# Kernel optimization log

Measured on AMD Instinct MI355X. Metric: run time of the kernel, lower is better.

Reference implementation:

```python
import jax, jax.numpy as jnp
import numpy as np

C = 512
NUM_HEADS = 8
GROUPS = 32
EPS = 1e-5


def setup_inputs() -> dict:
    key = jax.random.key(0)
    ks = jax.random.split(key, 7)
    B, H, W = 8, 32, 32
    x = jax.random.normal(ks[0], (B, C, H, W), dtype=jnp.float32)
    gn_w = jnp.ones((C,), dtype=jnp.float32)
    gn_b = jnp.zeros((C,), dtype=jnp.float32)
    # 1x1 convs as dense matrices [out, in]
    qkv_w = jax.random.normal(ks[1], (3 * C, C), dtype=jnp.float32) * (1.0 / np.sqrt(C))
    qkv_b = jnp.zeros((3 * C,), dtype=jnp.float32)
    proj_w = jax.random.normal(ks[2], (C, C), dtype=jnp.float32) * (1.0 / np.sqrt(C))
    proj_b = jnp.zeros((C,), dtype=jnp.float32)
    return {"x": x, "gn_w": gn_w, "gn_b": gn_b, "qkv_w": qkv_w,
            "qkv_b": qkv_b, "proj_w": proj_w, "proj_b": proj_b}


def reference(x, gn_w, gn_b, qkv_w, qkv_b, proj_w, proj_b):
    B, Cc, H, W = x.shape
    nh = NUM_HEADS
    d = Cc // nh
    N = H * W

    # GroupNorm(32, C) with affine
    xg = x.reshape(B, GROUPS, Cc // GROUPS, H, W)
    mean = jnp.mean(xg, axis=(2, 3, 4), keepdims=True)
    var = jnp.var(xg, axis=(2, 3, 4), keepdims=True)
    hn = ((xg - mean) * jax.lax.rsqrt(var + EPS)).reshape(B, Cc, H, W)
    hn = hn * gn_w[None, :, None, None] + gn_b[None, :, None, None]

    # 1x1 conv QKV projection: [B, 3C, H, W]
    qkv = jnp.einsum('oc,bchw->bohw', qkv_w, hn) + qkv_b[None, :, None, None]
    q, k, v = jnp.split(qkv, 3, axis=1)

    def to_heads(t):  # [B, C, H, W] -> [B, nh, N, d]
        return t.reshape(B, nh, d, N).transpose(0, 1, 3, 2)

    q, k, v = to_heads(q), to_heads(k), to_heads(v)
    scale = d ** (-0.5)
    attn = jax.nn.softmax(jnp.einsum('bhnd,bhmd->bhnm', q, k) * scale, axis=-1)
    o = jnp.einsum('bhnm,bhmd->bhnd', attn, v)          # [B, nh, N, d]
    o = o.transpose(0, 1, 3, 2).reshape(B, Cc, H, W)

    # 1x1 conv output projection + residual
    o = jnp.einsum('oc,bchw->bohw', proj_w, o) + proj_b[None, :, None, None]
    return x + o
```

## Files before the change

kernel.cpp:

```cpp
#include <hip/hip_runtime.h>

typedef __bf16 bf16x8 __attribute__((ext_vector_type(8)));
typedef float f32x4 __attribute__((ext_vector_type(4)));

#define MFMA(a, b, c) __builtin_amdgcn_mfma_f32_16x16x32_bf16(a, b, c, 0, 0, 0)

#define CS 0.18033688011112042f

__device__ __forceinline__ ushort f2bf(float f) {
    __bf16 h = (__bf16)f;
    return *(ushort*)&h;
}
__device__ __forceinline__ float bf2f(ushort u) {
    unsigned int x = ((unsigned int)u) << 16;
    return __uint_as_float(x);
}

__device__ __forceinline__ void stage_tile64(ushort* lds, const ushort* gbase,
                                             int row_stride, int nchunks,
                                             int wave, int lane) {
    int r8 = lane >> 3;
    int cswz = ((lane & 7) ^ r8) << 4;
#pragma unroll
    for (int c = wave; c < nchunks; c += 4) {
        const char* g = (const char*)(gbase + (size_t)(c * 8 + r8) * row_stride) + cswz;
        __builtin_amdgcn_global_load_lds(
            (const __attribute__((address_space(1))) unsigned int*)g,
            (__attribute__((address_space(3))) unsigned int*)((char*)lds + c * 1024),
            16, 0, 0);
    }
}

__device__ __forceinline__ void stage_tile64w2(ushort* lds, const ushort* gbase,
                                               int row_stride, int nchunks,
                                               int wave, int lane) {
    int r8 = lane >> 3;
    int cswz = ((lane & 7) ^ r8) << 4;
#pragma unroll
    for (int c = wave; c < nchunks; c += 2) {
        const char* g = (const char*)(gbase + (size_t)(c * 8 + r8) * row_stride) + cswz;
        __builtin_amdgcn_global_load_lds(
            (const __attribute__((address_space(1))) unsigned int*)g,
            (__attribute__((address_space(3))) unsigned int*)((char*)lds + c * 1024),
            16, 0, 0);
    }
}

__device__ __forceinline__ bf16x8 lds_read_row(const ushort* lds, int row, int cb) {
    return *(const bf16x8*)((const char*)lds + row * 128 + (cb ^ ((row & 7) << 4)));
}

__device__ __forceinline__ void stage_tile32(ushort* lds, const ushort* gbase,
                                             int row_stride, int nchunks,
                                             int wave, int lane) {
    int r16 = lane >> 2;
    int csw = (((lane & 3) ^ ((lane >> 3) & 3)) << 3);
#pragma unroll
    for (int c = wave; c < nchunks; c += 4) {
        const ushort* g = gbase + (size_t)(c * 16 + r16) * row_stride + csw;
        __builtin_amdgcn_global_load_lds(
            (const __attribute__((address_space(1))) unsigned int*)g,
            (__attribute__((address_space(3))) unsigned int*)((char*)lds + c * 1024),
            16, 0, 0);
    }
}

__device__ __forceinline__ bf16x8 lds_read_row32(const ushort* lds, int row, int cb) {
    return *(const bf16x8*)((const char*)lds + row * 64 + (cb ^ (((row >> 1) & 3) << 4)));
}

__global__ __launch_bounds__(256) void gn_cvt_kernel(const float* __restrict__ x,
                                                     const float* __restrict__ gnw,
                                                     const float* __restrict__ gnb,
                                                     ushort* __restrict__ hnT,
                                                     const float* __restrict__ w1,
                                                     const float* __restrict__ w2,
                                                     ushort* __restrict__ o1,
                                                     ushort* __restrict__ o2) {
    __shared__ ushort xcache[16 * 1028];
    __shared__ float red[8];
    __shared__ float sw[16], sb[16];

    if (blockIdx.x >= 256) {
        int t = (blockIdx.x - 256) * 256 + threadIdx.x;
        const int n1q = (1536 * 512) / 4;
        float4 v;
        ushort* dst;
        int idx;
        if (t < n1q) {
            v = ((const float4*)w1)[t]; dst = o1; idx = t;
        } else {
            idx = t - n1q;
            v = ((const float4*)w2)[idx]; dst = o2;
        }
        ushort4 p;
        p.x = f2bf(v.x); p.y = f2bf(v.y); p.z = f2bf(v.z); p.w = f2bf(v.w);
        ((ushort4*)dst)[idx] = p;
        return;
    }

    int b = blockIdx.x >> 5, g = blockIdx.x & 31;
    const float* xp = x + (size_t)(b * 512 + g * 16) * 1024;
    int t = threadIdx.x;

    float s = 0.f, ss = 0.f;
    const float4* xp4 = (const float4*)xp;
    for (int i = t; i < 4096; i += 256) {
        float4 v = xp4[i];
        s += (v.x + v.y) + (v.z + v.w);
        ss += (v.x * v.x + v.y * v.y) + (v.z * v.z + v.w * v.w);
        int f = i * 4;
        int cc = f >> 10, nl = f & 1023;
        ushort4 c;
        c.x = f2bf(v.x); c.y = f2bf(v.y); c.z = f2bf(v.z); c.w = f2bf(v.w);
        *(ushort4*)&xcache[cc * 1028 + nl] = c;
    }
#pragma unroll
    for (int off = 32; off >= 1; off >>= 1) {
        s += __shfl_xor(s, off);
        ss += __shfl_xor(ss, off);
    }
    int wave = t >> 6;
    if ((t & 63) == 0) { red[wave] = s; red[wave + 4] = ss; }
    if (t < 16) { sw[t] = gnw[g * 16 + t]; sb[t] = gnb[g * 16 + t]; }
    __syncthreads();
    float S = red[0] + red[1] + red[2] + red[3];
    float SS = red[4] + red[5] + red[6] + red[7];
    float mean = S * (1.0f / 16384.0f);
    float var = SS * (1.0f / 16384.0f) - mean * mean;
    float rstd = rsqrtf(var + 1e-5f);

    int cc0 = (t & 3) * 4;
    int nb = t >> 2;
    float w0 = sw[cc0] * rstd, w1_ = sw[cc0 + 1] * rstd,
          w2_ = sw[cc0 + 2] * rstd, w3 = sw[cc0 + 3] * rstd;
    float b0 = sb[cc0] - mean * w0, b1 = sb[cc0 + 1] - mean * w1_,
          b2 = sb[cc0 + 2] - mean * w2_, b3 = sb[cc0 + 3] - mean * w3;
#pragma unroll
    for (int k = 0; k < 16; ++k) {
        int nl = nb + 64 * k;
        ushort4 p;
        p.x = f2bf(bf2f(xcache[(cc0 + 0) * 1028 + nl]) * w0 + b0);
        p.y = f2bf(bf2f(xcache[(cc0 + 1) * 1028 + nl]) * w1_ + b1);
        p.z = f2bf(bf2f(xcache[(cc0 + 2) * 1028 + nl]) * w2_ + b2);
        p.w = f2bf(bf2f(xcache[(cc0 + 3) * 1028 + nl]) * w3 + b3);
        *(ushort4*)(hnT + ((size_t)b * 1024 + nl) * 512 + g * 16 + cc0) = p;
    }
}

__global__ __launch_bounds__(256, 3) void gemm_qkv(const ushort* __restrict__ Wb,
                                                   const ushort* __restrict__ hnT,
                                                   const float* __restrict__ qkvb,
                                                   ushort* __restrict__ qT,
                                                   ushort* __restrict__ kT,
                                                   ushort* __restrict__ vb) {
    int lane = threadIdx.x & 63, wave = threadIdx.x >> 6;
    int l15 = lane & 15, lg = lane >> 4;
    int bi = blockIdx.x;
    int b = bi & 7;
    int slot = bi >> 3;
    int m0 = (slot % 12) * 128;
    int n0 = (slot / 12) * 128;
    int mw = (wave >> 1) * 64, nw = (wave & 1) * 64;
    const ushort* Ag = Wb + (size_t)m0 * 512;
    const ushort* Bg = hnT + (size_t)b * 524288 + (size_t)n0 * 512;

    __shared__ ushort abuf[3][4096];
    __shared__ ushort bbuf[3][4096];

    f32x4 acc[4][4] = {};
#pragma unroll
    for (int p = 0; p < 2; ++p) {
        stage_tile32(abuf[p], Ag + p * 32, 512, 8, wave, lane);
        stage_tile32(bbuf[p], Bg + p * 32, 512, 8, wave, lane);
    }
    asm volatile("s_waitcnt vmcnt(4)" ::: "memory");
    __builtin_amdgcn_s_barrier();

    int cur = 0;
#pragma unroll 1
    for (int t = 0; t < 16; ++t) {
        if (t < 14) {
            int nxt = cur + 2; if (nxt >= 3) nxt -= 3;
            stage_tile32(abuf[nxt], Ag + (t + 2) * 32, 512, 8, wave, lane);
            stage_tile32(bbuf[nxt], Bg + (t + 2) * 32, 512, 8, wave, lane);
        }
        const ushort* A = abuf[cur];
        const ushort* B = bbuf[cur];
        bf16x8 af[4], bfr[4];
#pragma unroll
        for (int i = 0; i < 4; i++)
            af[i] = lds_read_row32(A, mw + i * 16 + l15, lg * 16);
#pragma unroll
        for (int j = 0; j < 4; j++)
            bfr[j] = lds_read_row32(B, nw + j * 16 + l15, lg * 16);
        __builtin_amdgcn_s_setprio(1);
#pragma unroll
        for (int i = 0; i < 4; i++)
#pragma unroll
            for (int j = 0; j < 4; j++)
                acc[i][j] = MFMA(af[i], bfr[j], acc[i][j]);
        __builtin_amdgcn_s_setprio(0);
        if (t < 15) {
            if (t < 14) asm volatile("s_waitcnt vmcnt(4)" ::: "memory");
            else        asm volatile("s_waitcnt vmcnt(0)" ::: "memory");
            __builtin_amdgcn_s_barrier();
        }
        cur = cur + 1; if (cur == 3) cur = 0;
    }

#pragma unroll
    for (int i = 0; i < 4; i++) {
        int ob = m0 + mw + i * 16 + lg * 4;
        float bias[4];
#pragma unroll
        for (int r = 0; r < 4; r++) bias[r] = qkvb[ob + r];
        int part = ob >> 9;
        int oo = ob & 511;
#pragma unroll
        for (int j = 0; j < 4; j++) {
            int n = n0 + nw + j * 16 + l15;
            if (part == 2) {
                int L = n & 63;
                int cf = L >> 4;
                int s = ((cf >> 1) << 5) | (((L >> 2) & 3) << 3) | ((cf & 1) << 2) | (L & 3);
                int np = (n & ~63) | s;
#pragma unroll
                for (int r = 0; r < 4; r++)
                    vb[(size_t)(b * 512 + oo + r) * 1024 + np] = f2bf(acc[i][j][r] + bias[r]);
            } else {
                ushort* dst = part ? kT : qT;
                float sc = part ? 1.0f : CS;
                int h = oo >> 6, dd = oo & 63;
                ushort4 p;
                p.x = f2bf((acc[i][j][0] + bias[0]) * sc);
                p.y = f2bf((acc[i][j][1] + bias[1]) * sc);
                p.z = f2bf((acc[i][j][2] + bias[2]) * sc);
                p.w = f2bf((acc[i][j][3] + bias[3]) * sc);
                *(ushort4*)(dst + ((size_t)((b * 8 + h) * 1024 + n)) * 64 + dd) = p;
            }
        }
    }
}

__global__ __launch_bounds__(128) void attn_kernel(const ushort* __restrict__ qT,
                                                   const ushort* __restrict__ kT,
                                                   const ushort* __restrict__ vb,
                                                   ushort* __restrict__ aoT) {
    int bi = blockIdx.x;
    int bh = ((bi >> 6) << 3) | (bi & 7);
    int q0 = ((bi >> 3) & 7) * 128;
    int b = bh >> 3, h = bh & 7;
    int lane = threadIdx.x & 63, wave = threadIdx.x >> 6;
    int l15 = lane & 15, lg = lane >> 4;
    const ushort* qp = qT + (size_t)bh * 65536;
    const ushort* kp = kT + (size_t)bh * 65536;
    const ushort* vp = vb + (size_t)bh * 65536;

    __shared__ ushort kbuf[3][4096];
    __shared__ ushort vbuf[3][4096];

    bf16x8 vone;
#pragma unroll
    for (int e = 0; e < 8; e++) vone[e] = (__bf16)1.0f;

    int qbase = q0 + wave * 64;
    bf16x8 qf[4][2];
#pragma unroll
    for (int i = 0; i < 4; i++)
#pragma unroll
        for (int kh = 0; kh < 2; kh++)
            qf[i][kh] = *(const bf16x8*)(qp + (size_t)(qbase + i * 16 + l15) * 64 + kh * 32 + lg * 8);

    f32x4 oacc[4][4] = {};
    f32x4 lacc[4] = {};

    stage_tile64w2(kbuf[0], kp, 64, 8, wave, lane);
    stage_tile64w2(vbuf[0], vp, 1024, 8, wave, lane);
    stage_tile64w2(kbuf[1], kp + 4096, 64, 8, wave, lane);
    stage_tile64w2(vbuf[1], vp + 64, 1024, 8, wave, lane);
    asm volatile("s_waitcnt vmcnt(8)" ::: "memory");
    __builtin_amdgcn_s_barrier();

    int cur = 0;
#pragma unroll 1
    for (int t = 0; t < 16; ++t) {
        if (t < 14) {
            int nxt = cur + 2; if (nxt >= 3) nxt -= 3;
            stage_tile64w2(kbuf[nxt], kp + (size_t)(t + 2) * 4096, 64, 8, wave, lane);
            stage_tile64w2(vbuf[nxt], vp + (t + 2) * 64, 1024, 8, wave, lane);
        }
        const ushort* kb = kbuf[cur];
        const ushort* vc = vbuf[cur];

        bf16x8 kf[2][4], vf[2][4];
#pragma unroll
        for (int kh = 0; kh < 2; kh++)
#pragma unroll
            for (int cf = 0; cf < 4; cf++)
                kf[kh][cf] = lds_read_row(kb, cf * 16 + l15, kh * 64 + lg * 16);
#pragma unroll
        for (int ks = 0; ks < 2; ks++)
#pragma unroll
            for (int cf = 0; cf < 4; cf++)
                vf[ks][cf] = lds_read_row(vc, cf * 16 + l15, ks * 64 + lg * 16);

#pragma unroll
        for (int ih = 0; ih < 2; ih++) {
            f32x4 sacc[2][4] = {};
            __builtin_amdgcn_s_setprio(1);
#pragma unroll
            for (int kh = 0; kh < 2; kh++)
#pragma unroll
                for (int cf = 0; cf < 4; cf++) {
                    sacc[0][cf] = MFMA(kf[kh][cf], qf[2 * ih + 0][kh], sacc[0][cf]);
                    sacc[1][cf] = MFMA(kf[kh][cf], qf[2 * ih + 1][kh], sacc[1][cf]);
                }
            __builtin_amdgcn_s_setprio(0);

            bf16x8 pa[2][2];
#pragma unroll
            for (int ii = 0; ii < 2; ii++)
#pragma unroll
                for (int ks = 0; ks < 2; ks++) {
                    bf16x8 tr;
#pragma unroll
                    for (int jhi = 0; jhi < 2; jhi++)
#pragma unroll
                        for (int r = 0; r < 4; r++)
                            tr[jhi * 4 + r] = (__bf16)exp2f(sacc[ii][ks * 2 + jhi][r]);
                    pa[ii][ks] = tr;
                }

            __builtin_amdgcn_s_setprio(1);
#pragma unroll
            for (int ii = 0; ii < 2; ii++)
#pragma unroll
                for (int ks = 0; ks < 2; ks++) {
                    lacc[2 * ih + ii] = MFMA(pa[ii][ks], vone, lacc[2 * ih + ii]);
#pragma unroll
                    for (int cf = 0; cf < 4; cf++)
                        oacc[2 * ih + ii][cf] = MFMA(pa[ii][ks], vf[ks][cf], oacc[2 * ih + ii][cf]);
                }
            __builtin_amdgcn_s_setprio(0);
        }

        if (t < 15) {
            if (t < 14) asm volatile("s_waitcnt vmcnt(8)" ::: "memory");
            else        asm volatile("s_waitcnt vmcnt(0)" ::: "memory");
            __builtin_amdgcn_s_barrier();
        }
        cur = cur + 1; if (cur == 3) cur = 0;
    }

#pragma unroll
    for (int i = 0; i < 4; i++)
#pragma unroll
        for (int r = 0; r < 4; r++) {
            float inv = 1.0f / lacc[i][r];
            int n = qbase + i * 16 + lg * 4 + r;
            size_t obase = ((size_t)b * 1024 + n) * 512 + h * 64;
#pragma unroll
            for (int cf = 0; cf < 4; cf++)
                aoT[obase + cf * 16 + l15] = f2bf(oacc[i][cf][r] * inv);
        }
}

__global__ __launch_bounds__(256) void gemm_proj(const ushort* __restrict__ Wb,
                                                 const ushort* __restrict__ aoT,
                                                 const float* __restrict__ projb,
                                                 const float* __restrict__ x,
                                                 float* __restrict__ out) {
    int lane = threadIdx.x & 63, wave = threadIdx.x >> 6;
    int l15 = lane & 15, lg = lane >> 4;
    int bi = blockIdx.x;
    int b = bi & 7;
    int slot = bi >> 3;
    int m0 = (slot & 3) * 128;
    int n0 = (slot >> 2) * 64;
    int mw = (wave >> 1) * 64, nw = (wave & 1) * 32;
    const ushort* Ag = Wb + (size_t)m0 * 512;
    const ushort* Bg = aoT + (size_t)b * 524288 + (size_t)n0 * 512;

    __shared__ ushort abuf[4][4096];
    __shared__ ushort bbuf[4][2048];

    f32x4 acc[4][2] = {};
#pragma unroll
    for (int p = 0; p < 3; ++p) {
        stage_tile32(abuf[p], Ag + p * 32, 512, 8, wave, lane);
        stage_tile32(bbuf[p], Bg + p * 32, 512, 4, wave, lane);
    }
    asm volatile("s_waitcnt vmcnt(6)" ::: "memory");
    __builtin_amdgcn_s_barrier();

#pragma unroll 1
    for (int t = 0; t < 16; ++t) {
        if (t < 13) {
            int nxt = (t + 3) & 3;
            stage_tile32(abuf[nxt], Ag + (t + 3) * 32, 512, 8, wave, lane);
            stage_tile32(bbuf[nxt], Bg + (t + 3) * 32, 512, 4, wave, lane);
        }
        const ushort* A = abuf[t & 3];
        const ushort* B = bbuf[t & 3];
        bf16x8 af[4], bfr[2];
#pragma unroll
        for (int i = 0; i < 4; i++)
            af[i] = lds_read_row32(A, mw + i * 16 + l15, lg * 16);
#pragma unroll
        for (int j = 0; j < 2; j++)
            bfr[j] = lds_read_row32(B, nw + j * 16 + l15, lg * 16);
        __builtin_amdgcn_s_setprio(1);
#pragma unroll
        for (int i = 0; i < 4; i++)
#pragma unroll
            for (int j = 0; j < 2; j++)
                acc[i][j] = MFMA(af[i], bfr[j], acc[i][j]);
        __builtin_amdgcn_s_setprio(0);
        if (t < 15) {
            if (t < 13)      asm volatile("s_waitcnt vmcnt(6)" ::: "memory");
            else if (t == 13) asm volatile("s_waitcnt vmcnt(3)" ::: "memory");
            else              asm volatile("s_waitcnt vmcnt(0)" ::: "memory");
            __builtin_amdgcn_s_barrier();
        }
    }

#pragma unroll
    for (int i = 0; i < 4; i++) {
        int ob = m0 + mw + i * 16 + lg * 4;
        float bias[4];
#pragma unroll
        for (int r = 0; r < 4; r++) bias[r] = projb[ob + r];
#pragma unroll
        for (int j = 0; j < 2; j++) {
            int n = n0 + nw + j * 16 + l15;
#pragma unroll
            for (int r = 0; r < 4; r++) {
                size_t idx = (size_t)(b * 512 + ob + r) * 1024 + n;
                out[idx] = x[idx] + bias[r] + acc[i][j][r];
            }
        }
    }
}

extern "C" void kernel_launch(void* const* d_in, const int* in_sizes, int n_in,
                              void* d_out, int out_size, void* d_ws, size_t ws_size,
                              hipStream_t stream) {
    const float* x     = (const float*)d_in[0];
    const float* gnw   = (const float*)d_in[1];
    const float* gnb   = (const float*)d_in[2];
    const float* qkvw  = (const float*)d_in[3];
    const float* qkvb  = (const float*)d_in[4];
    const float* projw = (const float*)d_in[5];
    const float* projb = (const float*)d_in[6];
    float* out = (float*)d_out;

    char* ws = (char*)d_ws;
    ushort* hnT    = (ushort*)(ws);
    ushort* qT     = (ushort*)(ws + (size_t)(8u << 20));
    ushort* kT     = (ushort*)(ws + (size_t)(16u << 20));
    ushort* vbuf   = (ushort*)(ws + (size_t)(24u << 20));
    ushort* qkvwb  = (ushort*)(ws + (size_t)(32u << 20));
    ushort* projwb = (ushort*)(ws + (size_t)(32u << 20) + 1572864);

    gn_cvt_kernel<<<dim3(1280), dim3(256), 0, stream>>>(x, gnw, gnb, hnT,
                                                        qkvw, projw, qkvwb, projwb);
    gemm_qkv<<<dim3(768), dim3(256), 0, stream>>>(qkvwb, hnT, qkvb, qT, kT, vbuf);
    attn_kernel<<<dim3(512), dim3(128), 0, stream>>>(qT, kT, vbuf, hnT );
    gemm_proj<<<dim3(512), dim3(256), 0, stream>>>(projwb, hnT, projb, x, out);
}
```

Baseline: 87.37 us.

## Split KV range across wave pairs in attention and combine partials through LDS

```diff
diff --git a/kernel.cpp b/kernel.cpp
--- a/kernel.cpp
+++ b/kernel.cpp
@@ -23,21 +23,6 @@
     int cswz = ((lane & 7) ^ r8) << 4;
 #pragma unroll
     for (int c = wave; c < nchunks; c += 4) {
-        const char* g = (const char*)(gbase + (size_t)(c * 8 + r8) * row_stride) + cswz;
-        __builtin_amdgcn_global_load_lds(
-            (const __attribute__((address_space(1))) unsigned int*)g,
-            (__attribute__((address_space(3))) unsigned int*)((char*)lds + c * 1024),
-            16, 0, 0);
-    }
-}
-
-__device__ __forceinline__ void stage_tile64w2(ushort* lds, const ushort* gbase,
-                                               int row_stride, int nchunks,
-                                               int wave, int lane) {
-    int r8 = lane >> 3;
-    int cswz = ((lane & 7) ^ r8) << 4;
-#pragma unroll
-    for (int c = wave; c < nchunks; c += 2) {
         const char* g = (const char*)(gbase + (size_t)(c * 8 + r8) * row_stride) + cswz;
         __builtin_amdgcn_global_load_lds(
             (const __attribute__((address_space(1))) unsigned int*)g,
@@ -243,7 +228,7 @@
     }
 }
 
-__global__ __launch_bounds__(128) void attn_kernel(const ushort* __restrict__ qT,
+__global__ __launch_bounds__(256) void attn_kernel(const ushort* __restrict__ qT,
                                                    const ushort* __restrict__ kT,
                                                    const ushort* __restrict__ vb,
                                                    ushort* __restrict__ aoT) {
@@ -253,18 +238,21 @@
     int b = bh >> 3, h = bh & 7;
     int lane = threadIdx.x & 63, wave = threadIdx.x >> 6;
     int l15 = lane & 15, lg = lane >> 4;
+    int qg = wave & 1, kvh = wave >> 1;
     const ushort* qp = qT + (size_t)bh * 65536;
     const ushort* kp = kT + (size_t)bh * 65536;
     const ushort* vp = vb + (size_t)bh * 65536;
 
-    __shared__ ushort kbuf[3][4096];
-    __shared__ ushort vbuf[3][4096];
+    __shared__ char smem[65536];
+    ushort* kbuf = (ushort*)smem;
+    ushort* vbuf = (ushort*)(smem + 32768);
+    float*  comb = (float*)smem;
 
     bf16x8 vone;
 #pragma unroll
     for (int e = 0; e < 8; e++) vone[e] = (__bf16)1.0f;
 
-    int qbase = q0 + wave * 64;
+    int qbase = q0 + qg * 64;
     bf16x8 qf[4][2];
 #pragma unroll
     for (int i = 0; i < 4; i++)
@@ -275,23 +263,25 @@
     f32x4 oacc[4][4] = {};
     f32x4 lacc[4] = {};
 
-    stage_tile64w2(kbuf[0], kp, 64, 8, wave, lane);
-    stage_tile64w2(vbuf[0], vp, 1024, 8, wave, lane);
-    stage_tile64w2(kbuf[1], kp + 4096, 64, 8, wave, lane);
-    stage_tile64w2(vbuf[1], vp + 64, 1024, 8, wave, lane);
-    asm volatile("s_waitcnt vmcnt(8)" ::: "memory");
+    stage_tile64(kbuf, kp, 64, 8, wave, lane);
+    stage_tile64(vbuf, vp, 1024, 8, wave, lane);
+    stage_tile64(kbuf + 4096, kp + 4096, 64, 8, wave, lane);
+    stage_tile64(vbuf + 4096, vp + 64, 1024, 8, wave, lane);
+    asm volatile("s_waitcnt vmcnt(0)" ::: "memory");
     __builtin_amdgcn_s_barrier();
 
-    int cur = 0;
 #pragma unroll 1
-    for (int t = 0; t < 16; ++t) {
-        if (t < 14) {
-            int nxt = cur + 2; if (nxt >= 3) nxt -= 3;
-            stage_tile64w2(kbuf[nxt], kp + (size_t)(t + 2) * 4096, 64, 8, wave, lane);
-            stage_tile64w2(vbuf[nxt], vp + (t + 2) * 64, 1024, 8, wave, lane);
-        }
-        const ushort* kb = kbuf[cur];
-        const ushort* vc = vbuf[cur];
+    for (int s = 0; s < 8; ++s) {
+        if (s < 7) {
+            int t2 = 2 * s + 2, t3 = 2 * s + 3;
+            stage_tile64(kbuf + (t2 & 3) * 4096, kp + (size_t)t2 * 4096, 64, 8, wave, lane);
+            stage_tile64(vbuf + (t2 & 3) * 4096, vp + t2 * 64, 1024, 8, wave, lane);
+            stage_tile64(kbuf + (t3 & 3) * 4096, kp + (size_t)t3 * 4096, 64, 8, wave, lane);
+            stage_tile64(vbuf + (t3 & 3) * 4096, vp + t3 * 64, 1024, 8, wave, lane);
+        }
+        int t = 2 * s + kvh;
+        const ushort* kb = kbuf + (t & 3) * 4096;
+        const ushort* vc = vbuf + (t & 3) * 4096;
 
         bf16x8 kf[2][4], vf[2][4];
 #pragma unroll
@@ -345,25 +335,48 @@
             __builtin_amdgcn_s_setprio(0);
         }
 
-        if (t < 15) {
-            if (t < 14) asm volatile("s_waitcnt vmcnt(8)" ::: "memory");
-            else        asm volatile("s_waitcnt vmcnt(0)" ::: "memory");
+        if (s < 7) {
+            asm volatile("s_waitcnt vmcnt(0)" ::: "memory");
             __builtin_amdgcn_s_barrier();
         }
-        cur = cur + 1; if (cur == 3) cur = 0;
-    }
-
-#pragma unroll
-    for (int i = 0; i < 4; i++)
-#pragma unroll
-        for (int r = 0; r < 4; r++) {
-            float inv = 1.0f / lacc[i][r];
-            int n = qbase + i * 16 + lg * 4 + r;
-            size_t obase = ((size_t)b * 1024 + n) * 512 + h * 64;
+    }
+
+    __builtin_amdgcn_s_barrier();
+    if (kvh == 1) {
+        float* dst = comb + qg * 5120;
+#pragma unroll
+        for (int i = 0; i < 4; i++)
 #pragma unroll
             for (int cf = 0; cf < 4; cf++)
-                aoT[obase + cf * 16 + l15] = f2bf(oacc[i][cf][r] * inv);
-        }
+                *(f32x4*)(dst + (i * 4 + cf) * 256 + lane * 4) = oacc[i][cf];
+#pragma unroll
+        for (int i = 0; i < 4; i++)
+            *(f32x4*)(dst + (16 + i) * 256 + lane * 4) = lacc[i];
+    }
+    __builtin_amdgcn_s_barrier();
+    if (kvh == 0) {
+        const float* src = comb + qg * 5120;
+#pragma unroll
+        for (int i = 0; i < 4; i++)
+#pragma unroll
+            for (int cf = 0; cf < 4; cf++)
+                oacc[i][cf] += *(const f32x4*)(src + (i * 4 + cf) * 256 + lane * 4);
+#pragma unroll
+        for (int i = 0; i < 4; i++)
+            lacc[i] += *(const f32x4*)(src + (16 + i) * 256 + lane * 4);
+
+#pragma unroll
+        for (int i = 0; i < 4; i++)
+#pragma unroll
+            for (int r = 0; r < 4; r++) {
+                float inv = 1.0f / lacc[i][r];
+                int n = qbase + i * 16 + lg * 4 + r;
+                size_t obase = ((size_t)b * 1024 + n) * 512 + h * 64;
+#pragma unroll
+                for (int cf = 0; cf < 4; cf++)
+                    aoT[obase + cf * 16 + l15] = f2bf(oacc[i][cf][r] * inv);
+            }
+    }
 }
 
 __global__ __launch_bounds__(256) void gemm_proj(const ushort* __restrict__ Wb,
@@ -466,6 +479,6 @@
     gn_cvt_kernel<<<dim3(1280), dim3(256), 0, stream>>>(x, gnw, gnb, hnT,
                                                         qkvw, projw, qkvwb, projwb);
     gemm_qkv<<<dim3(768), dim3(256), 0, stream>>>(qkvwb, hnT, qkvb, qT, kT, vbuf);
-    attn_kernel<<<dim3(512), dim3(128), 0, stream>>>(qT, kT, vbuf, hnT );
+    attn_kernel<<<dim3(512), dim3(256), 0, stream>>>(qT, kT, vbuf, hnT );
     gemm_proj<<<dim3(512), dim3(256), 0, stream>>>(projwb, hnT, projb, x, out);
 }
```

Result: slower. 90.76 us (+3.9%).
